# Optimization experiments

Hardware: AMD Instinct MI355X
Metric: run time of the kernel (lower is better)

Reference implementation:

```python
import jax, jax.numpy as jnp
import numpy as np

B, N, FP, TP = 4, 64, 256, 32
V, D = 32000, 1024


def setup_inputs() -> dict:
    key = jax.random.key(0)
    k1, k2, k3 = jax.random.split(key, 3)
    x_prime = jax.random.normal(k1, (B, N, FP, TP), dtype=jnp.float32)
    token_embedding = jax.random.normal(k2, (V, D), dtype=jnp.float32) * 0.02
    # xavier_uniform for W: bound = sqrt(6/(F'+V))
    bound = np.sqrt(6.0 / (FP + V)).astype(np.float32)
    W = jax.random.uniform(k3, (FP, V), dtype=jnp.float32, minval=-bound, maxval=bound)
    b = jnp.zeros((V,), dtype=jnp.float32)
    return {"x_prime": x_prime, "token_embedding": token_embedding, "W": W, "b": b}


def reference(x_prime, token_embedding, W, b):
    # x_prime: (B, N, F', T') -> permute(0,3,1,2) -> (B, T', N, F') -> (B, L, F'), L = N*T'
    Bb, Nn, Fp, Tp = x_prime.shape
    x_flat = jnp.transpose(x_prime, (0, 3, 1, 2)).reshape(Bb, Nn * Tp, Fp)
    # logits: (B, L, V); temperature == 1.0 so no division
    logits = jnp.einsum('blf,fv->blv', x_flat, W) + b
    P = jax.nn.softmax(logits, axis=-1)          # (B, L, V)
    H_graph = jnp.einsum('blv,vd->bld', P, token_embedding)  # (B, L, d_model)
    return H_graph
```

## Files before the change

kernel.cpp:

```cpp
#include <hip/hip_runtime.h>
#include <cstdint>
#include <cstddef>

typedef __bf16 bf16_t;
typedef __bf16 bf16x8 __attribute__((ext_vector_type(8)));
typedef float f32x4 __attribute__((ext_vector_type(4)));

#define B_  4
#define N_  64
#define FP_ 256
#define TP_ 32
#define V_  32000
#define D_  1024
#define L_  2048
#define M_  8192
#define VT_ 125

__device__ __forceinline__ void async_copy16(const void* g, void* l) {
  __builtin_amdgcn_global_load_lds(
      (__attribute__((address_space(1))) void*)g,
      (__attribute__((address_space(3))) void*)l,
      16, 0, 0);
}

__global__ __launch_bounds__(256) void k_convert_x(const float* __restrict__ xp,
                                                   bf16_t* __restrict__ Xb) {
  __shared__ float tile[256][33];
  const int tid = threadIdx.x;
  const int b = blockIdx.x >> 6;
  const int n = blockIdx.x & 63;
  const float* src = xp + (size_t)(b * N_ + n) * FP_ * TP_;
#pragma unroll
  for (int i = 0; i < 32; i++) {
    int idx = i * 256 + tid;
    tile[idx >> 5][idx & 31] = src[idx];
  }
  __syncthreads();
#pragma unroll
  for (int t = 0; t < 32; t++) {
    Xb[(size_t)(b * L_ + t * N_ + n) * FP_ + tid] = (bf16_t)tile[tid][t];
  }
}

__global__ void k_transpose_cvt(const float* __restrict__ src, bf16_t* __restrict__ dst,
                                int R, int C) {
  __shared__ float tile[64][65];
  int ct = blockIdx.x;
  int rt = blockIdx.y;
  int tid = threadIdx.x;
#pragma unroll
  for (int i = 0; i < 16; i++) {
    int idx = tid + i * 256;
    int a = idx >> 6, bc = idx & 63;
    tile[a][bc] = src[(size_t)(rt * 64 + a) * C + ct * 64 + bc];
  }
  __syncthreads();
#pragma unroll
  for (int i = 0; i < 16; i++) {
    int idx = tid + i * 256;
    int a = idx >> 6, bc = idx & 63;
    dst[(size_t)(ct * 64 + a) * R + rt * 64 + bc] = (bf16_t)tile[bc][a];
  }
}

#define BAR() asm volatile("s_barrier" ::: "memory")
#define VMW(n) asm volatile("s_waitcnt vmcnt(" #n ")" ::: "memory")
#define LGW(n) asm volatile("s_waitcnt lgkmcnt(" #n ")" ::: "memory")

__global__ __launch_bounds__(512, 2) void k_gemm1(
    const bf16_t* __restrict__ Xb, const bf16_t* __restrict__ Wt,
    const float* __restrict__ bias, bf16_t* __restrict__ P,
    float* __restrict__ rs_part, int mbase) {
  __shared__ __align__(16) bf16_t smem[65536];

  const int tid = threadIdx.x;
  const int lane = tid & 63;
  const int wid = tid >> 6;
  const int wm = wid >> 2;
  const int wn = wid & 3;
  const int c16 = lane & 15, quad = lane >> 4;

  const int nwg = (int)gridDim.x;
  const int q = nwg >> 3, r = nwg & 7;
  const int xcd = blockIdx.x & 7, bidx = (int)blockIdx.x >> 3;
  const int vb = (xcd < r) ? xcd * (q + 1) + bidx : r + xcd * q + bidx;
  const int vtile = vb % VT_;
  const int mtile = vb / VT_;

  const int v0 = vtile * 256;
  const int prow0 = mtile * 256;
  const int m0 = mbase + prow0;

  const int l3 = lane >> 3;
  const int cA = (lane & 7) ^ l3;
  const int grA = (l3 << 1) + (cA >> 2);
  const int gcA = (cA & 3) << 3;
  const int rA0 = (wid & 4) * 32 + (wid & 3) * 16;
  const int rB0 = (wid >> 1) * 64 + (wid & 1) * 16;

  const bf16_t* gA = Xb + (size_t)(m0 + grA) * FP_ + gcA;
  const bf16_t* gB = Wt + (size_t)(v0 + grA) * FP_ + gcA;

  float bv[4];
#pragma unroll
  for (int J = 0; J < 4; J++)
    bv[J] = bias[v0 + wn * 64 + (J >> 1) * 32 + (J & 1) * 16 + c16];

  f32x4 acc[8][4];
#pragma unroll
  for (int i = 0; i < 8; i++)
#pragma unroll
    for (int j = 0; j < 4; j++) acc[i][j] = (f32x4){0.f, 0.f, 0.f, 0.f};

  bf16x8 af[4][2], bfr[2][2];

#define G1_STAGE_A(buf, t, half)                                        \
  do {                                                                  \
    int r0_ = rA0 + (half) * 64;                                        \
    const bf16_t* s_ = gA + (size_t)r0_ * FP_ + (t) * 64;               \
    async_copy16(s_,      &smem[((buf) * 2 + 0) * 8192 + r0_ * 32]);    \
    async_copy16(s_ + 32, &smem[((buf) * 2 + 1) * 8192 + r0_ * 32]);    \
  } while (0)
#define G1_STAGE_B(buf, t, half)                                        \
  do {                                                                  \
    int r0_ = rB0 + (half) * 32;                                        \
    const bf16_t* s_ = gB + (size_t)r0_ * FP_ + (t) * 64;               \
    async_copy16(s_,      &smem[32768 + ((buf) * 2 + 0) * 8192 + r0_ * 32]); \
    async_copy16(s_ + 32, &smem[32768 + ((buf) * 2 + 1) * 8192 + r0_ * 32]); \
  } while (0)
#define G1_READ_A(buf, mh)                                              \
  do {                                                                  \
    _Pragma("unroll")                                                   \
    for (int i_ = 0; i_ < 4; i_++) {                                    \
      int r_ = wm * 128 + (mh) * 64 + i_ * 16 + c16;                    \
      int pa_ = r_ >> 1;                                                \
      int cz_ = ((((r_ & 1) << 2) | quad) ^ (pa_ & 7)) << 3;            \
      af[i_][0] = *(const bf16x8*)&smem[((buf) * 2 + 0) * 8192 + pa_ * 64 + cz_]; \
      af[i_][1] = *(const bf16x8*)&smem[((buf) * 2 + 1) * 8192 + pa_ * 64 + cz_]; \
    }                                                                   \
  } while (0)
#define G1_READ_B(buf, nh)                                              \
  do {                                                                  \
    _Pragma("unroll")                                                   \
    for (int j_ = 0; j_ < 2; j_++) {                                    \
      int r_ = wn * 64 + (nh) * 32 + j_ * 16 + c16;                     \
      int pn_ = r_ >> 1;                                                \
      int cz_ = ((((r_ & 1) << 2) | quad) ^ (pn_ & 7)) << 3;            \
      bfr[j_][0] = *(const bf16x8*)&smem[32768 + ((buf) * 2 + 0) * 8192 + pn_ * 64 + cz_]; \
      bfr[j_][1] = *(const bf16x8*)&smem[32768 + ((buf) * 2 + 1) * 8192 + pn_ * 64 + cz_]; \
    }                                                                   \
  } while (0)
#define G1_MFMA16(mh, nh)                                               \
  do {                                                                  \
    __builtin_amdgcn_s_setprio(1);                                      \
    _Pragma("unroll")                                                   \
    for (int i_ = 0; i_ < 4; i_++)                                      \
      _Pragma("unroll")                                                 \
      for (int j_ = 0; j_ < 2; j_++) {                                  \
        acc[(mh)*4 + i_][(nh)*2 + j_] = __builtin_amdgcn_mfma_f32_16x16x32_bf16( \
            af[i_][0], bfr[j_][0], acc[(mh)*4 + i_][(nh)*2 + j_], 0, 0, 0);      \
        acc[(mh)*4 + i_][(nh)*2 + j_] = __builtin_amdgcn_mfma_f32_16x16x32_bf16( \
            af[i_][1], bfr[j_][1], acc[(mh)*4 + i_][(nh)*2 + j_], 0, 0, 0);      \
      }                                                                 \
    __builtin_amdgcn_s_setprio(0);                                      \
  } while (0)

  G1_STAGE_A(0, 0, 0); G1_STAGE_B(0, 0, 0); G1_STAGE_B(0, 0, 1); G1_STAGE_A(0, 0, 1);
  VMW(0);
  BAR();

  const int NT = 4;
#pragma unroll
  for (int t = 0; t < NT; ++t) {
    const int cur = t & 1, nb = cur ^ 1;
    const bool pf = (t + 1 < NT);

    G1_READ_A(cur, 0); G1_READ_B(cur, 0);
    if (pf) G1_STAGE_A(nb, t + 1, 0);
    LGW(8);
    BAR();
    LGW(0);
    G1_MFMA16(0, 0);
    if (pf) VMW(4); else VMW(2);
    BAR();

    G1_READ_B(cur, 1);
    if (pf) G1_STAGE_B(nb, t + 1, 0);
    BAR();
    LGW(0);
    G1_MFMA16(0, 1);
    if (pf) VMW(4); else VMW(0);
    BAR();

    G1_READ_A(cur, 1);
    if (pf) G1_STAGE_B(nb, t + 1, 1);
    BAR();
    LGW(0);
    G1_MFMA16(1, 1);
    BAR();

    G1_READ_B(cur, 0);
    if (pf) G1_STAGE_A(nb, t + 1, 1);
    BAR();
    LGW(0);
    G1_MFMA16(1, 0);
    if (pf) {
      VMW(4);
      BAR();
    }
  }

#pragma unroll
  for (int I = 0; I < 8; I++) {
    int rowb = wm * 128 + (I >> 2) * 64 + (I & 3) * 16;
#pragma unroll
    for (int e = 0; e < 4; e++) {
      int row = rowb + quad * 4 + e;
      float s = 0.0f;
#pragma unroll
      for (int J = 0; J < 4; J++) {
        float p = __expf(acc[I][J][e] + bv[J]);
        float pf32 = (float)(bf16_t)p;
        acc[I][J][e] = pf32;
        s += pf32;
      }
#pragma unroll
      for (int off = 1; off < 16; off <<= 1) s += __shfl_xor(s, off, 16);
      if (c16 == 0)
        rs_part[(size_t)(prow0 + row) * 512 + vtile * 4 + wn] = s;
    }
  }

  __syncthreads();
#pragma unroll
  for (int I = 0; I < 8; I++) {
    int rowb = wm * 128 + (I >> 2) * 64 + (I & 3) * 16;
#pragma unroll
    for (int e = 0; e < 4; e++) {
      int row = rowb + quad * 4 + e;
#pragma unroll
      for (int J = 0; J < 4; J++) {
        int ch = wn * 8 + (J >> 1) * 4 + (J & 1) * 2 + (c16 >> 3);
        smem[row * 256 + ((ch ^ (row & 7)) << 3) + (c16 & 7)] = (bf16_t)acc[I][J][e];
      }
    }
  }
  __syncthreads();
#pragma unroll
  for (int it = 0; it < 16; it++) {
    int idx2 = it * 512 + tid;
    int row = idx2 >> 5, ch = idx2 & 31;
    *(bf16x8*)&P[(size_t)(prow0 + row) * V_ + v0 + ch * 8] =
        *(const bf16x8*)&smem[row * 256 + ((ch ^ (row & 7)) << 3)];
  }
#undef G1_STAGE_A
#undef G1_STAGE_B
#undef G1_READ_A
#undef G1_READ_B
#undef G1_MFMA16
}

__global__ void k_rowsum_reduce(const float* __restrict__ rs_part,
                                float* __restrict__ rowsum, int mbase) {
  int row = blockIdx.x * 4 + (threadIdx.x >> 6);
  int lane = threadIdx.x & 63;
  float s = 0.0f;
  for (int j = lane; j < VT_ * 4; j += 64) s += rs_part[(size_t)row * 512 + j];
#pragma unroll
  for (int off = 32; off >= 1; off >>= 1) s += __shfl_xor(s, off, 64);
  if (lane == 0) rowsum[mbase + row] = s;
}

__global__ __launch_bounds__(512, 2) void k_gemm2(
    const bf16_t* __restrict__ P, const bf16_t* __restrict__ Et,
    float* __restrict__ partial, int mtiles, int chunkrows, int kper) {
  __shared__ __align__(16) bf16_t ldsA[2][2][8192];
  __shared__ __align__(16) bf16_t ldsB[2][2][8192];

  const int tid = threadIdx.x;
  const int lane = tid & 63;
  const int wid = tid >> 6;
  const int wm = wid >> 2;
  const int wn = wid & 3;
  const int c16 = lane & 15, quad = lane >> 4;

  const int nwg = (int)gridDim.x;
  const int xcd = blockIdx.x & 7;
  const int vb = xcd * (nwg >> 3) + ((int)blockIdx.x >> 3);
  const int dtile = vb & 3;
  const int rest = vb >> 2;
  const int mtile = rest % mtiles;
  const int kslice = rest / mtiles;

  const int d0 = dtile * 256;
  const int prow0 = mtile * 256;
  const int kbase = kslice * kper;
  float* __restrict__ o = partial + (size_t)kslice * chunkrows * D_;

  const int l3 = lane >> 3;
  const int cA = (lane & 7) ^ l3;
  const int grA = (l3 << 1) + (cA >> 2);
  const int gcA = (cA & 3) << 3;

  const int rA0 = (wid & 4) * 32 + (wid & 3) * 16;
  const int rB0 = (wid >> 1) * 64 + (wid & 1) * 16;

  const bf16_t* gA = P  + (size_t)(prow0 + grA) * V_ + kbase + gcA;
  const bf16_t* gB = Et + (size_t)(d0   + grA) * V_ + kbase + gcA;

  f32x4 acc[8][4];
#pragma unroll
  for (int i = 0; i < 8; i++)
#pragma unroll
    for (int j = 0; j < 4; j++) acc[i][j] = (f32x4){0.f, 0.f, 0.f, 0.f};

  bf16x8 af[4][2], bfr[2][2];

#define STAGE_A(buf, t, half)                                          \
  do {                                                                 \
    int r0_ = rA0 + (half) * 64;                                       \
    const bf16_t* s_ = gA + (size_t)r0_ * V_ + (t) * 64;               \
    async_copy16(s_,      &ldsA[buf][0][r0_ * 32]);                    \
    async_copy16(s_ + 32, &ldsA[buf][1][r0_ * 32]);                    \
  } while (0)
#define STAGE_B(buf, t, half)                                          \
  do {                                                                 \
    int r0_ = rB0 + (half) * 32;                                       \
    const bf16_t* s_ = gB + (size_t)r0_ * V_ + (t) * 64;               \
    async_copy16(s_,      &ldsB[buf][0][r0_ * 32]);                    \
    async_copy16(s_ + 32, &ldsB[buf][1][r0_ * 32]);                    \
  } while (0)
#define READ_A(buf, mh)                                                \
  do {                                                                 \
    _Pragma("unroll")                                                  \
    for (int i_ = 0; i_ < 4; i_++) {                                   \
      int r_ = wm * 128 + (mh) * 64 + i_ * 16 + c16;                   \
      int pa_ = r_ >> 1;                                               \
      int cz_ = ((((r_ & 1) << 2) | quad) ^ (pa_ & 7)) << 3;           \
      af[i_][0] = *(const bf16x8*)&ldsA[buf][0][pa_ * 64 + cz_];       \
      af[i_][1] = *(const bf16x8*)&ldsA[buf][1][pa_ * 64 + cz_];       \
    }                                                                  \
  } while (0)
#define READ_B(buf, nh)                                                \
  do {                                                                 \
    _Pragma("unroll")                                                  \
    for (int j_ = 0; j_ < 2; j_++) {                                   \
      int r_ = wn * 64 + (nh) * 32 + j_ * 16 + c16;                    \
      int pn_ = r_ >> 1;                                               \
      int cz_ = ((((r_ & 1) << 2) | quad) ^ (pn_ & 7)) << 3;           \
      bfr[j_][0] = *(const bf16x8*)&ldsB[buf][0][pn_ * 64 + cz_];      \
      bfr[j_][1] = *(const bf16x8*)&ldsB[buf][1][pn_ * 64 + cz_];      \
    }                                                                  \
  } while (0)
#define MFMA16(mh, nh)                                                 \
  do {                                                                 \
    __builtin_amdgcn_s_setprio(1);                                     \
    _Pragma("unroll")                                                  \
    for (int i_ = 0; i_ < 4; i_++)                                     \
      _Pragma("unroll")                                                \
      for (int j_ = 0; j_ < 2; j_++) {                                 \
        acc[(mh)*4 + i_][(nh)*2 + j_] = __builtin_amdgcn_mfma_f32_16x16x32_bf16( \
            af[i_][0], bfr[j_][0], acc[(mh)*4 + i_][(nh)*2 + j_], 0, 0, 0);      \
        acc[(mh)*4 + i_][(nh)*2 + j_] = __builtin_amdgcn_mfma_f32_16x16x32_bf16( \
            af[i_][1], bfr[j_][1], acc[(mh)*4 + i_][(nh)*2 + j_], 0, 0, 0);      \
      }                                                                \
    __builtin_amdgcn_s_setprio(0);                                     \
  } while (0)

  STAGE_A(0, 0, 0); STAGE_B(0, 0, 0); STAGE_B(0, 0, 1); STAGE_A(0, 0, 1);
  VMW(4);
  BAR();

  const int NT = kper >> 6;
  for (int t = 0; t < NT; ++t) {
    const int cur = t & 1, nb = cur ^ 1;
    const bool pf = (t + 1 < NT);

    READ_A(cur, 0); READ_B(cur, 0);
    if (pf) STAGE_A(nb, t + 1, 0);
    LGW(8);
    BAR();
    LGW(0);
    MFMA16(0, 0);
    if (pf) VMW(4); else VMW(2);
    BAR();

    READ_B(cur, 1);
    if (pf) STAGE_B(nb, t + 1, 0);
    BAR();
    LGW(0);
    MFMA16(0, 1);
    if (pf) VMW(4); else VMW(0);
    BAR();

    READ_A(cur, 1);
    if (pf) STAGE_B(nb, t + 1, 1);
    BAR();
    LGW(0);
    MFMA16(1, 1);
    BAR();

    READ_B(cur, 0);
    if (pf) STAGE_A(nb, t + 1, 1);
    BAR();
    LGW(0);
    MFMA16(1, 0);
    if (pf) {
      VMW(4);
      BAR();
    }
  }

#pragma unroll
  for (int I = 0; I < 8; I++) {
    int rowb = wm * 128 + (I >> 2) * 64 + (I & 3) * 16;
#pragma unroll
    for (int e = 0; e < 4; e++) {
      int pr = prow0 + rowb + quad * 4 + e;
#pragma unroll
      for (int J = 0; J < 4; J++) {
        int d = d0 + wn * 64 + (J >> 1) * 32 + (J & 1) * 16 + c16;
        o[(size_t)pr * D_ + d] = acc[I][J][e];
      }
    }
  }
#undef STAGE_A
#undef STAGE_B
#undef READ_A
#undef READ_B
#undef MFMA16
}

#undef BAR
#undef VMW
#undef LGW

__global__ void k_finalize(const float* __restrict__ partial,
                           const float* __restrict__ rowsum, float* __restrict__ out,
                           int mbase, int rows, int ks) {
  int i = blockIdx.x * 256 + threadIdx.x;
  int lr = i >> 8;
  float inv = 1.0f / rowsum[mbase + lr];
  f32x4 s = (f32x4){0.f, 0.f, 0.f, 0.f};
  for (int z = 0; z < ks; z++) {
    f32x4 a = ((const f32x4*)(partial + (size_t)z * rows * D_))[i];
    s.x += a.x; s.y += a.y; s.z += a.z; s.w += a.w;
  }
  s.x *= inv; s.y *= inv; s.z *= inv; s.w *= inv;
  ((f32x4*)out)[(size_t)mbase * (D_ / 4) + i] = s;
}

extern "C" void kernel_launch(void* const* d_in, const int* in_sizes, int n_in,
                              void* d_out, int out_size, void* d_ws, size_t ws_size,
                              hipStream_t stream) {
  const float* xp   = (const float*)d_in[0];
  const float* E    = (const float*)d_in[1];
  const float* W    = (const float*)d_in[2];
  const float* bias = (const float*)d_in[3];
  float* out = (float*)d_out;

  char* ws = (char*)d_ws;
  const size_t szXb = (size_t)M_ * FP_ * 2;
  const size_t szWt = (size_t)V_ * FP_ * 2;
  const size_t szEt = (size_t)D_ * V_ * 2;
  const size_t szRs = (size_t)M_ * 4;
  bf16_t* Xb = (bf16_t*)ws;
  bf16_t* Wt = (bf16_t*)(ws + szXb);
  bf16_t* Et = (bf16_t*)(ws + szXb + szWt);
  float* rowsum = (float*)(ws + szXb + szWt + szEt);
  const size_t fixed = szXb + szWt + szEt + szRs;

  const int copt[4] = {8192, 4096, 2048, 1024};
  const int kopt[4] = {2, 4, 10, 20};
  int chunk = 1024, ksv = 20;
  size_t avail = (ws_size > fixed) ? ws_size - fixed : 0;
  for (int i = 0; i < 4; i++) {
    size_t need = (size_t)copt[i] * V_ * 2 + (size_t)kopt[i] * copt[i] * D_ * 4
                + (size_t)copt[i] * 512 * 4;
    if (need <= avail) { chunk = copt[i]; ksv = kopt[i]; break; }
  }
  bf16_t* P = (bf16_t*)(ws + fixed);
  float* partial = (float*)(ws + fixed + (size_t)chunk * V_ * 2);
  float* rs_part = (float*)(ws + fixed + (size_t)chunk * V_ * 2
                            + (size_t)ksv * chunk * D_ * 4);
  const int kper = V_ / ksv;

  k_convert_x<<<B_ * N_, 256, 0, stream>>>(xp, Xb);
  {
    dim3 g(V_ / 64, FP_ / 64);
    k_transpose_cvt<<<g, 256, 0, stream>>>(W, Wt, FP_, V_);
  }
  {
    dim3 g(D_ / 64, V_ / 64);
    k_transpose_cvt<<<g, 256, 0, stream>>>(E, Et, V_, D_);
  }

  for (int mb = 0; mb < M_; mb += chunk) {
    int rows = M_ - mb;
    if (rows > chunk) rows = chunk;

    int nwg1 = VT_ * (rows / 256);
    k_gemm1<<<nwg1, 512, 0, stream>>>(Xb, Wt, bias, P, rs_part, mb);
    k_rowsum_reduce<<<rows / 4, 256, 0, stream>>>(rs_part, rowsum, mb);

    int mt = rows / 256;
    int nwg2 = 4 * mt * ksv;
    k_gemm2<<<nwg2, 512, 0, stream>>>(P, Et, partial, mt, rows, kper);

    k_finalize<<<rows, 256, 0, stream>>>(partial, rowsum, out, mb, rows, ksv);
  }
}
```

Measured before the change: 1.181 ms.

## Restructure P·E GEMM loop with register double-buffered fragments and fewer barriers

Rewrites the main loop of the P×E^T MFMA kernel. The A and B fragments are now held in two register sets, so the next tile's first fragments are read from LDS while the current tile's MFMAs are still running. All loads for a K-tile are issued up front and the number of workgroup barriers per iteration drops from about eight to two. Quadrant ordering is simplified so MFMAs iterate over k-halves on the outside. The cost is more VGPRs for the doubled fragment buffers, which may reduce occupancy, and a tighter reliance on the vmcnt-based wait logic for LDS safety.

```diff
diff --git a/kernel.cpp b/kernel.cpp
--- a/kernel.cpp
+++ b/kernel.cpp
@@ -314,7 +314,7 @@
 #pragma unroll
     for (int j = 0; j < 4; j++) acc[i][j] = (f32x4){0.f, 0.f, 0.f, 0.f};
 
-  bf16x8 af[4][2], bfr[2][2];
+  bf16x8 afm0[4][2], afm1[4][2], bB0[2][2], bB1[2][2];
 
 #define STAGE_A(buf, t, half)                                          \
   do {                                                                 \
@@ -330,105 +330,89 @@
     async_copy16(s_,      &ldsB[buf][0][r0_ * 32]);                    \
     async_copy16(s_ + 32, &ldsB[buf][1][r0_ * 32]);                    \
   } while (0)
-#define READ_A(buf, mh)                                                \
-  do {                                                                 \
-    _Pragma("unroll")                                                  \
+#define LDSOFF(r_) (((r_) >> 1) * 64 + (((((r_) & 1) << 2) | quad) ^ (((r_) >> 1) & 7)) * 8)
+#define READ_A_HALF(buf, base_i, dst)                                  \
+  do { _Pragma("unroll")                                               \
     for (int i_ = 0; i_ < 4; i_++) {                                   \
-      int r_ = wm * 128 + (mh) * 64 + i_ * 16 + c16;                   \
-      int pa_ = r_ >> 1;                                               \
-      int cz_ = ((((r_ & 1) << 2) | quad) ^ (pa_ & 7)) << 3;           \
-      af[i_][0] = *(const bf16x8*)&ldsA[buf][0][pa_ * 64 + cz_];       \
-      af[i_][1] = *(const bf16x8*)&ldsA[buf][1][pa_ * 64 + cz_];       \
-    }                                                                  \
-  } while (0)
-#define READ_B(buf, nh)                                                \
-  do {                                                                 \
-    _Pragma("unroll")                                                  \
+      int r_ = wm * 128 + ((base_i) + i_) * 16 + c16;                  \
+      int off_ = LDSOFF(r_);                                           \
+      dst[i_][0] = *(const bf16x8*)&ldsA[buf][0][off_];                \
+      dst[i_][1] = *(const bf16x8*)&ldsA[buf][1][off_];                \
+    } } while (0)
+#define READ_B_PAIR(buf, base_j, dst)                                  \
+  do { _Pragma("unroll")                                               \
     for (int j_ = 0; j_ < 2; j_++) {                                   \
-      int r_ = wn * 64 + (nh) * 32 + j_ * 16 + c16;                    \
-      int pn_ = r_ >> 1;                                               \
-      int cz_ = ((((r_ & 1) << 2) | quad) ^ (pn_ & 7)) << 3;           \
-      bfr[j_][0] = *(const bf16x8*)&ldsB[buf][0][pn_ * 64 + cz_];      \
-      bfr[j_][1] = *(const bf16x8*)&ldsB[buf][1][pn_ * 64 + cz_];      \
-    }                                                                  \
-  } while (0)
-#define MFMA16(mh, nh)                                                 \
+      int r_ = wn * 64 + ((base_j) + j_) * 16 + c16;                   \
+      int off_ = LDSOFF(r_);                                           \
+      dst[j_][0] = *(const bf16x8*)&ldsB[buf][0][off_];                \
+      dst[j_][1] = *(const bf16x8*)&ldsB[buf][1][off_];                \
+    } } while (0)
+#define Q_MFMA(bi, bj, AF, BF)                                         \
   do {                                                                 \
     __builtin_amdgcn_s_setprio(1);                                     \
     _Pragma("unroll")                                                  \
-    for (int i_ = 0; i_ < 4; i_++)                                     \
+    for (int kk_ = 0; kk_ < 2; kk_++)                                  \
       _Pragma("unroll")                                                \
-      for (int j_ = 0; j_ < 2; j_++) {                                 \
-        acc[(mh)*4 + i_][(nh)*2 + j_] = __builtin_amdgcn_mfma_f32_16x16x32_bf16( \
-            af[i_][0], bfr[j_][0], acc[(mh)*4 + i_][(nh)*2 + j_], 0, 0, 0);      \
-        acc[(mh)*4 + i_][(nh)*2 + j_] = __builtin_amdgcn_mfma_f32_16x16x32_bf16( \
-            af[i_][1], bfr[j_][1], acc[(mh)*4 + i_][(nh)*2 + j_], 0, 0, 0);      \
-      }                                                                \
+      for (int i_ = 0; i_ < 4; i_++)                                   \
+        _Pragma("unroll")                                              \
+        for (int j_ = 0; j_ < 2; j_++)                                 \
+          acc[(bi) + i_][(bj) + j_] =                                  \
+            __builtin_amdgcn_mfma_f32_16x16x32_bf16(                   \
+              AF[i_][kk_], BF[j_][kk_], acc[(bi) + i_][(bj) + j_], 0, 0, 0); \
     __builtin_amdgcn_s_setprio(0);                                     \
   } while (0)
 
-  STAGE_A(0, 0, 0); STAGE_B(0, 0, 0); STAGE_B(0, 0, 1); STAGE_A(0, 0, 1);
-  VMW(4);
+  STAGE_A(0, 0, 0); STAGE_A(0, 0, 1); STAGE_B(0, 0, 0); STAGE_B(0, 0, 1);
+  VMW(0);
   BAR();
+  READ_A_HALF(0, 0, afm0);
+  READ_B_PAIR(0, 0, bB0);
 
   const int NT = kper >> 6;
   for (int t = 0; t < NT; ++t) {
     const int cur = t & 1, nb = cur ^ 1;
     const bool pf = (t + 1 < NT);
 
-    READ_A(cur, 0); READ_B(cur, 0);
-    if (pf) STAGE_A(nb, t + 1, 0);
-    LGW(8);
-    BAR();
-    LGW(0);
-    MFMA16(0, 0);
-    if (pf) VMW(4); else VMW(2);
-    BAR();
-
-    READ_B(cur, 1);
-    if (pf) STAGE_B(nb, t + 1, 0);
-    BAR();
-    LGW(0);
-    MFMA16(0, 1);
-    if (pf) VMW(4); else VMW(0);
-    BAR();
-
-    READ_A(cur, 1);
-    if (pf) STAGE_B(nb, t + 1, 1);
-    BAR();
-    LGW(0);
-    MFMA16(1, 1);
-    BAR();
-
-    READ_B(cur, 0);
-    if (pf) STAGE_A(nb, t + 1, 1);
-    BAR();
-    LGW(0);
-    MFMA16(1, 0);
+    if (pf) { STAGE_A(nb, t + 1, 0); STAGE_A(nb, t + 1, 1); }
+    READ_B_PAIR(cur, 2, bB1);
+    Q_MFMA(0, 0, afm0, bB0);
+
+    if (pf) { STAGE_B(nb, t + 1, 0); STAGE_B(nb, t + 1, 1); }
+    READ_A_HALF(cur, 4, afm1);
+    Q_MFMA(0, 2, afm0, bB1);
+
+    Q_MFMA(4, 2, afm1, bB1);
+    READ_B_PAIR(cur, 0, bB1);
+    VMW(2);
+    BAR();
+
+    if (pf) { READ_A_HALF(nb, 0, afm0); READ_B_PAIR(nb, 0, bB0); }
+    Q_MFMA(4, 0, afm1, bB1);
     if (pf) {
-      VMW(4);
+      VMW(0);
       BAR();
     }
   }
 
 #pragma unroll
   for (int I = 0; I < 8; I++) {
-    int rowb = wm * 128 + (I >> 2) * 64 + (I & 3) * 16;
+    int rowb = wm * 128 + I * 16;
 #pragma unroll
     for (int e = 0; e < 4; e++) {
       int pr = prow0 + rowb + quad * 4 + e;
 #pragma unroll
       for (int J = 0; J < 4; J++) {
-        int d = d0 + wn * 64 + (J >> 1) * 32 + (J & 1) * 16 + c16;
+        int d = d0 + wn * 64 + J * 16 + c16;
         o[(size_t)pr * D_ + d] = acc[I][J][e];
       }
     }
   }
 #undef STAGE_A
 #undef STAGE_B
-#undef READ_A
-#undef READ_B
-#undef MFMA16
+#undef LDSOFF
+#undef READ_A_HALF
+#undef READ_B_PAIR
+#undef Q_MFMA
 }
 
 #undef BAR
```

New measurement: 1.216 ms. 1.03x slower.
